# Kernel tuning notes

Measured on AMD Instinct MI355X. Metric: run time of the kernel, lower is better.

Reference implementation:

```python
import jax, jax.numpy as jnp
import numpy as np

N = 2_097_152   # batched ODE RHS evaluation points
T = 10_000      # forcing time-series length (days)
H = 16          # MLP hidden width


def _step(x):
    # smooth Heaviside used throughout EXP-Hydro
    return (jnp.tanh(5.0 * x) + 1.0) * 0.5


def _mlp(x, W1, b1, W2, b2, W3, b3):
    h = jnp.tanh(x @ W1 + b1)
    h = jnp.tanh(h @ W2 + b2)
    return (h @ W3 + b3)[..., 0]


def setup_inputs() -> dict:
    key = jax.random.key(0)
    ks = jax.random.split(key, 16)
    ts = jnp.arange(T, dtype=jnp.float32)
    inp = {
        "t": jax.random.uniform(ks[0], (N,), jnp.float32) * (T - 1),
        "S_snow": jax.random.uniform(ks[1], (N,), jnp.float32) * 50.0,
        "S_water": jax.random.uniform(ks[2], (N,), jnp.float32) * 1000.0,
        "ts": ts,
        "precp_series": jax.random.uniform(ks[3], (T,), jnp.float32) * 20.0,
        "temp_series": jax.random.normal(ks[4], (T,), jnp.float32) * 10.0,
        "lday_series": 0.3 + 0.4 * jax.random.uniform(ks[5], (T,), jnp.float32),
        "etW1": jax.random.normal(ks[6], (3, H), jnp.float32) * (1.0 / np.sqrt(3)),
        "etb1": jnp.zeros((H,), jnp.float32),
        "etW2": jax.random.normal(ks[7], (H, H), jnp.float32) * (1.0 / np.sqrt(H)),
        "etb2": jnp.zeros((H,), jnp.float32),
        "etW3": jax.random.normal(ks[8], (H, 1), jnp.float32) * (1.0 / np.sqrt(H)),
        "etb3": jnp.zeros((1,), jnp.float32),
        "qW1": jax.random.normal(ks[9], (2, H), jnp.float32) * (1.0 / np.sqrt(2)),
        "qb1": jnp.zeros((H,), jnp.float32),
        "qW2": jax.random.normal(ks[10], (H, H), jnp.float32) * (1.0 / np.sqrt(H)),
        "qb2": jnp.zeros((H,), jnp.float32),
        "qW3": jax.random.normal(ks[11], (H, 1), jnp.float32) * (1.0 / np.sqrt(H)),
        "qb3": jnp.zeros((1,), jnp.float32),
        "Df": jnp.float32(2.674),
        "Tmax": jnp.float32(0.176),
        "Tmin": jnp.float32(-2.093),
    }
    return inp


def reference(t, S_snow, S_water, ts, precp_series, temp_series, lday_series,
              etW1, etb1, etW2, etb2, etW3, etb3,
              qW1, qb1, qW2, qb2, qW3, qb3,
              Df, Tmax, Tmin):
    # linear interpolation of forcings at query times t  -> [N]
    precp = jnp.interp(t, ts, precp_series)
    temp = jnp.interp(t, ts, temp_series)
    lday = jnp.interp(t, ts, lday_series)

    ET = _mlp(jnp.stack([S_snow, S_water, temp], axis=-1),
              etW1, etb1, etW2, etb2, etW3, etb3)          # [N]
    Q = _mlp(jnp.stack([S_water, precp], axis=-1),
             qW1, qb1, qW2, qb2, qW3, qb3)                 # [N]

    # bucket physics (M / Ps / Pr with smooth step)
    melt = _step(temp - Tmax) * _step(S_snow) * jnp.minimum(S_snow, Df * (temp - Tmax))
    Ps = _step(Tmin - temp) * precp   # snowfall
    Pr = _step(temp - Tmin) * precp   # rainfall
    sw = _step(S_water)

    dS_1 = Ps - melt
    dS_2 = Pr + melt - sw * lday * jnp.exp(ET) - sw * jnp.exp(Q)
    return (dS_1, dS_2)
```

## Files before the change

kernel.cpp:

```cpp
#include <hip/hip_runtime.h>
#include <math.h>

#define BLOCK 256

typedef _Float16 half4v __attribute__((ext_vector_type(4)));
typedef float    float4v __attribute__((ext_vector_type(4)));

__device__ __forceinline__ float fast_tanh(float x) {
    float e = __expf(2.0f * x);
    float r = __builtin_amdgcn_rcpf(e + 1.0f);
    return 1.0f - 2.0f * r;
}

__device__ __forceinline__ float stepf(float x) {
    return (fast_tanh(5.0f * x) + 1.0f) * 0.5f;
}

__global__ __launch_bounds__(BLOCK) void pack_forcings_kernel(
    const float* __restrict__ precp_s, const float* __restrict__ temp_s,
    const float* __restrict__ lday_s, float4* __restrict__ F, int T)
{
    int i = blockIdx.x * BLOCK + threadIdx.x;
    if (i < T) F[i] = make_float4(precp_s[i], temp_s[i], lday_s[i], 0.0f);
}

__global__ __launch_bounds__(BLOCK, 4) void exphydro_mfma_kernel(
    const float* __restrict__ t, const float* __restrict__ S_snow,
    const float* __restrict__ S_water,
    const float4* __restrict__ F,
    const float* __restrict__ etW1, const float* __restrict__ etb1,
    const float* __restrict__ etW2, const float* __restrict__ etb2,
    const float* __restrict__ etW3, const float* __restrict__ etb3,
    const float* __restrict__ qW1, const float* __restrict__ qb1,
    const float* __restrict__ qW2, const float* __restrict__ qb2,
    const float* __restrict__ qW3, const float* __restrict__ qb3,
    const float* __restrict__ pDf, const float* __restrict__ pTmax,
    const float* __restrict__ pTmin,
    float* __restrict__ out, int N, int T)
{
    const int lane = threadIdx.x & 63;
    const int hi   = lane >> 4;
    const int m    = lane & 15;
    const int wave = threadIdx.x >> 6;
    const int base = blockIdx.x * BLOCK + wave * 64;
    const int p    = base + lane;
    const int pc   = (p < N) ? p : (N - 1);

    half4v A1et, A1q, A2et, A2q, A3et, A3q;
    float4v C2et, C2q;
    #pragma unroll
    for (int j = 0; j < 4; j++) {
        int k = 4 * hi + j;
        float w1e = (k < 3) ? etW1[k * 16 + m] : ((k == 3) ? etb1[m] : 0.0f);
        float w1q = (k < 2) ? qW1 [k * 16 + m] : ((k == 2) ? qb1 [m] : 0.0f);
        A1et[j] = (_Float16)w1e;
        A1q [j] = (_Float16)w1q;
        A2et[j] = (_Float16)etW2[k * 16 + m];
        A2q [j] = (_Float16)qW2 [k * 16 + m];
        A3et[j] = (_Float16)((m == 0) ? etW3[k] : 0.0f);
        A3q [j] = (_Float16)((m == 0) ? qW3 [k] : 0.0f);
        C2et[j] = etb2[4 * hi + j];
        C2q [j] = qb2 [4 * hi + j];
    }

    const float Df   = pDf[0];
    const float Tmax = pTmax[0];
    const float Tmin = pTmin[0];
    const float b3et = etb3[0];
    const float b3q  = qb3[0];
    const float tmaxf = (float)(T - 1);
    const int   imax  = T - 2;

    float tv    = t[pc];
    float ssnow = S_snow[pc];
    float swat  = S_water[pc];

    float tc = fminf(fmaxf(tv, 0.0f), tmaxf);
    int i0 = (int)tc;
    i0 = (i0 > imax) ? imax : i0;
    float fr = tc - (float)i0;
    float4 f0 = F[i0];
    float4 f1 = F[i0 + 1];
    float precp = fmaf(fr, f1.x - f0.x, f0.x);
    float temp  = fmaf(fr, f1.y - f0.y, f0.y);
    float lday  = fmaf(fr, f1.z - f0.z, f0.z);

    const float4v zero4 = {0.0f, 0.0f, 0.0f, 0.0f};
    float et4[4], q4[4];

    #pragma unroll
    for (int g = 0; g < 4; g++) {
        const int src = (g << 4) | m;
        float ss = __shfl(ssnow, src, 64);
        float sw = __shfl(swat,  src, 64);
        float tp = __shfl(temp,  src, 64);
        float pr = __shfl(precp, src, 64);

        half4v B1et, B1q;
        B1et[0] = (_Float16)ss;  B1et[1] = (_Float16)sw;
        B1et[2] = (_Float16)tp;  B1et[3] = (_Float16)1.0f;
        B1q [0] = (_Float16)sw;  B1q [1] = (_Float16)pr;
        B1q [2] = (_Float16)1.0f; B1q[3] = (_Float16)0.0f;

        float4v d1e = __builtin_amdgcn_mfma_f32_16x16x16f16(A1et, B1et, zero4, 0, 0, 0);
        float4v d1q = __builtin_amdgcn_mfma_f32_16x16x16f16(A1q,  B1q,  zero4, 0, 0, 0);

        half4v B2et, B2q;
        #pragma unroll
        for (int r = 0; r < 4; r++) B2et[r] = (_Float16)fast_tanh(d1e[r]);
        #pragma unroll
        for (int r = 0; r < 4; r++) B2q [r] = (_Float16)fast_tanh(d1q[r]);

        float4v d2e = __builtin_amdgcn_mfma_f32_16x16x16f16(A2et, B2et, C2et, 0, 0, 0);
        float4v d2q = __builtin_amdgcn_mfma_f32_16x16x16f16(A2q,  B2q,  C2q,  0, 0, 0);

        half4v B3et, B3q;
        #pragma unroll
        for (int r = 0; r < 4; r++) B3et[r] = (_Float16)fast_tanh(d2e[r]);
        #pragma unroll
        for (int r = 0; r < 4; r++) B3q [r] = (_Float16)fast_tanh(d2q[r]);

        float4v d3e = __builtin_amdgcn_mfma_f32_16x16x16f16(A3et, B3et, zero4, 0, 0, 0);
        float4v d3q = __builtin_amdgcn_mfma_f32_16x16x16f16(A3q,  B3q,  zero4, 0, 0, 0);

        et4[g] = d3e[0];
        q4 [g] = d3q[0];
    }

    float e0 = __shfl(et4[0], m, 64);
    float e1 = __shfl(et4[1], m, 64);
    float e2 = __shfl(et4[2], m, 64);
    float e3 = __shfl(et4[3], m, 64);
    float q0 = __shfl(q4[0], m, 64);
    float q1 = __shfl(q4[1], m, 64);
    float q2 = __shfl(q4[2], m, 64);
    float q3 = __shfl(q4[3], m, 64);
    float e01 = (lane & 16) ? e1 : e0;
    float e23 = (lane & 16) ? e3 : e2;
    float ET  = ((lane & 32) ? e23 : e01) + b3et;
    float q01 = (lane & 16) ? q1 : q0;
    float q23 = (lane & 16) ? q3 : q2;
    float Q   = ((lane & 32) ? q23 : q01) + b3q;

    float dT      = temp - Tmax;
    float melt    = stepf(dT) * stepf(ssnow) * fminf(ssnow, Df * dT);
    float st_snow = stepf(Tmin - temp);
    float Ps      = st_snow * precp;
    float Pr      = (1.0f - st_snow) * precp;
    float sw01    = stepf(swat);

    float dS1 = Ps - melt;
    float dS2 = Pr + melt - sw01 * (lday * __expf(ET) + __expf(Q));

    if (p < N) {
        out[p]     = dS1;
        out[N + p] = dS2;
    }
}

extern "C" void kernel_launch(void* const* d_in, const int* in_sizes, int n_in,
                              void* d_out, int out_size, void* d_ws, size_t ws_size,
                              hipStream_t stream) {
    const float* t        = (const float*)d_in[0];
    const float* S_snow   = (const float*)d_in[1];
    const float* S_water  = (const float*)d_in[2];
    const float* precp_s  = (const float*)d_in[4];
    const float* temp_s   = (const float*)d_in[5];
    const float* lday_s   = (const float*)d_in[6];
    const float* etW1     = (const float*)d_in[7];
    const float* etb1     = (const float*)d_in[8];
    const float* etW2     = (const float*)d_in[9];
    const float* etb2     = (const float*)d_in[10];
    const float* etW3     = (const float*)d_in[11];
    const float* etb3     = (const float*)d_in[12];
    const float* qW1      = (const float*)d_in[13];
    const float* qb1      = (const float*)d_in[14];
    const float* qW2      = (const float*)d_in[15];
    const float* qb2      = (const float*)d_in[16];
    const float* qW3      = (const float*)d_in[17];
    const float* qb3      = (const float*)d_in[18];
    const float* pDf      = (const float*)d_in[19];
    const float* pTmax    = (const float*)d_in[20];
    const float* pTmin    = (const float*)d_in[21];

    int N = in_sizes[0];
    int T = in_sizes[3];
    float* out = (float*)d_out;
    float4* F = (float4*)d_ws;

    pack_forcings_kernel<<<(T + BLOCK - 1) / BLOCK, BLOCK, 0, stream>>>(
        precp_s, temp_s, lday_s, F, T);

    exphydro_mfma_kernel<<<(N + BLOCK - 1) / BLOCK, BLOCK, 0, stream>>>(
        t, S_snow, S_water, F,
        etW1, etb1, etW2, etb2, etW3, etb3,
        qW1, qb1, qW2, qb2, qW3, qb3,
        pDf, pTmax, pTmin, out, N, T);
}
```

Measured before the change: 49.31 us.

## Use packed fp16 polynomial tanh and broadcast layer-3 weights to drop shuffles

Replaces the exp+rcp tanh with a clamped odd polynomial evaluated in packed fp16 vectors, for both the MLP activations and the smooth step functions. Inputs are packed to fp16 pairs before the wave shuffles, which halves the shuffle count. The layer-3 weights are broadcast across all MFMA rows and the bias is folded into the accumulator, so every lane receives its output directly and the final gather shuffles go away. The risk is accuracy: the fp16 polynomial with clamp at ±3 approximates tanh less closely, which matters most for the step functions on large physical inputs.

```diff
diff --git a/kernel.cpp b/kernel.cpp
--- a/kernel.cpp
+++ b/kernel.cpp
@@ -3,17 +3,51 @@
 
 #define BLOCK 256
 
+typedef _Float16 half2v __attribute__((ext_vector_type(2)));
 typedef _Float16 half4v __attribute__((ext_vector_type(4)));
 typedef float    float4v __attribute__((ext_vector_type(4)));
 
-__device__ __forceinline__ float fast_tanh(float x) {
-    float e = __expf(2.0f * x);
-    float r = __builtin_amdgcn_rcpf(e + 1.0f);
-    return 1.0f - 2.0f * r;
-}
-
-__device__ __forceinline__ float stepf(float x) {
-    return (fast_tanh(5.0f * x) + 1.0f) * 0.5f;
+__device__ __forceinline__ half2v cvt_pk_h2(float a, float b) {
+    return __builtin_bit_cast(half2v, __builtin_amdgcn_cvt_pkrtz(a, b));
+}
+
+#define H4(x) {(_Float16)(x), (_Float16)(x), (_Float16)(x), (_Float16)(x)}
+
+__device__ __forceinline__ half4v tanh_pk4(half4v x) {
+    const half4v c5 = H4(-3.71625e-05f);
+    const half4v c4 = H4( 1.09648e-03f);
+    const half4v c3 = H4(-1.288264e-02f);
+    const half4v c2 = H4( 7.941906e-02f);
+    const half4v c1 = H4(-3.0042735e-01f);
+    const half4v c0 = H4( 9.9607644e-01f);
+    const half4v hi = H4( 3.0f);
+    const half4v lo = H4(-3.0f);
+    half4v t = __builtin_elementwise_min(__builtin_elementwise_max(x, lo), hi);
+    half4v s = t * t;
+#if __has_builtin(__builtin_elementwise_fma)
+    half4v p = __builtin_elementwise_fma(c5, s, c4);
+    p = __builtin_elementwise_fma(p, s, c3);
+    p = __builtin_elementwise_fma(p, s, c2);
+    p = __builtin_elementwise_fma(p, s, c1);
+    p = __builtin_elementwise_fma(p, s, c0);
+#else
+    half4v p = c5 * s + c4;
+    p = p * s + c3;
+    p = p * s + c2;
+    p = p * s + c1;
+    p = p * s + c0;
+#endif
+    return t * p;
+}
+
+__device__ __forceinline__ half4v pk4_from_f32(float a, float b, float c, float d) {
+    half2v lo = cvt_pk_h2(a, b);
+    half2v hi = cvt_pk_h2(c, d);
+    return __builtin_shufflevector(lo, hi, 0, 1, 2, 3);
+}
+
+__device__ __forceinline__ half4v act4(float4v d) {
+    return tanh_pk4(pk4_from_f32(d[0], d[1], d[2], d[3]));
 }
 
 __global__ __launch_bounds__(BLOCK) void pack_forcings_kernel(
@@ -47,7 +81,7 @@
     const int pc   = (p < N) ? p : (N - 1);
 
     half4v A1et, A1q, A2et, A2q, A3et, A3q;
-    float4v C2et, C2q;
+    float4v C2et, C2q, C3et, C3q;
     #pragma unroll
     for (int j = 0; j < 4; j++) {
         int k = 4 * hi + j;
@@ -57,17 +91,17 @@
         A1q [j] = (_Float16)w1q;
         A2et[j] = (_Float16)etW2[k * 16 + m];
         A2q [j] = (_Float16)qW2 [k * 16 + m];
-        A3et[j] = (_Float16)((m == 0) ? etW3[k] : 0.0f);
-        A3q [j] = (_Float16)((m == 0) ? qW3 [k] : 0.0f);
+        A3et[j] = (_Float16)etW3[k];
+        A3q [j] = (_Float16)qW3 [k];
         C2et[j] = etb2[4 * hi + j];
         C2q [j] = qb2 [4 * hi + j];
+        C3et[j] = etb3[0];
+        C3q [j] = qb3 [0];
     }
 
     const float Df   = pDf[0];
     const float Tmax = pTmax[0];
     const float Tmin = pTmin[0];
-    const float b3et = etb3[0];
-    const float b3q  = qb3[0];
     const float tmaxf = (float)(T - 1);
     const int   imax  = T - 2;
 
@@ -85,69 +119,67 @@
     float temp  = fmaf(fr, f1.y - f0.y, f0.y);
     float lday  = fmaf(fr, f1.z - f0.z, f0.z);
 
+    half2v my01 = cvt_pk_h2(ssnow, swat);
+    half2v my23 = cvt_pk_h2(temp, precp);
+    int i01 = __builtin_bit_cast(int, my01);
+    int i23 = __builtin_bit_cast(int, my23);
+
     const float4v zero4 = {0.0f, 0.0f, 0.0f, 0.0f};
-    float et4[4], q4[4];
+    const _Float16 oneh = (_Float16)1.0f;
+    const _Float16 zerh = (_Float16)0.0f;
+    float et0, et1, et2, et3, q0, q1, q2, q3;
 
     #pragma unroll
     for (int g = 0; g < 4; g++) {
         const int src = (g << 4) | m;
-        float ss = __shfl(ssnow, src, 64);
-        float sw = __shfl(swat,  src, 64);
-        float tp = __shfl(temp,  src, 64);
-        float pr = __shfl(precp, src, 64);
-
-        half4v B1et, B1q;
-        B1et[0] = (_Float16)ss;  B1et[1] = (_Float16)sw;
-        B1et[2] = (_Float16)tp;  B1et[3] = (_Float16)1.0f;
-        B1q [0] = (_Float16)sw;  B1q [1] = (_Float16)pr;
-        B1q [2] = (_Float16)1.0f; B1q[3] = (_Float16)0.0f;
+        int j01 = __shfl(i01, src, 64);
+        int j23 = __shfl(i23, src, 64);
+        half2v a01 = __builtin_bit_cast(half2v, j01);
+        half2v a23 = __builtin_bit_cast(half2v, j23);
+
+        half4v B1et = {a01[0], a01[1], a23[0], oneh};
+        half4v B1q  = {a01[1], a23[1], oneh,  zerh};
 
         float4v d1e = __builtin_amdgcn_mfma_f32_16x16x16f16(A1et, B1et, zero4, 0, 0, 0);
         float4v d1q = __builtin_amdgcn_mfma_f32_16x16x16f16(A1q,  B1q,  zero4, 0, 0, 0);
 
-        half4v B2et, B2q;
-        #pragma unroll
-        for (int r = 0; r < 4; r++) B2et[r] = (_Float16)fast_tanh(d1e[r]);
-        #pragma unroll
-        for (int r = 0; r < 4; r++) B2q [r] = (_Float16)fast_tanh(d1q[r]);
+        half4v B2et = act4(d1e);
+        half4v B2q  = act4(d1q);
 
         float4v d2e = __builtin_amdgcn_mfma_f32_16x16x16f16(A2et, B2et, C2et, 0, 0, 0);
         float4v d2q = __builtin_amdgcn_mfma_f32_16x16x16f16(A2q,  B2q,  C2q,  0, 0, 0);
 
-        half4v B3et, B3q;
-        #pragma unroll
-        for (int r = 0; r < 4; r++) B3et[r] = (_Float16)fast_tanh(d2e[r]);
-        #pragma unroll
-        for (int r = 0; r < 4; r++) B3q [r] = (_Float16)fast_tanh(d2q[r]);
-
-        float4v d3e = __builtin_amdgcn_mfma_f32_16x16x16f16(A3et, B3et, zero4, 0, 0, 0);
-        float4v d3q = __builtin_amdgcn_mfma_f32_16x16x16f16(A3q,  B3q,  zero4, 0, 0, 0);
-
-        et4[g] = d3e[0];
-        q4 [g] = d3q[0];
+        half4v B3et = act4(d2e);
+        half4v B3q  = act4(d2q);
+
+        float4v d3e = __builtin_amdgcn_mfma_f32_16x16x16f16(A3et, B3et, C3et, 0, 0, 0);
+        float4v d3q = __builtin_amdgcn_mfma_f32_16x16x16f16(A3q,  B3q,  C3q,  0, 0, 0);
+
+        if (g == 0) { et0 = d3e[0]; q0 = d3q[0]; }
+        if (g == 1) { et1 = d3e[0]; q1 = d3q[0]; }
+        if (g == 2) { et2 = d3e[0]; q2 = d3q[0]; }
+        if (g == 3) { et3 = d3e[0]; q3 = d3q[0]; }
     }
 
-    float e0 = __shfl(et4[0], m, 64);
-    float e1 = __shfl(et4[1], m, 64);
-    float e2 = __shfl(et4[2], m, 64);
-    float e3 = __shfl(et4[3], m, 64);
-    float q0 = __shfl(q4[0], m, 64);
-    float q1 = __shfl(q4[1], m, 64);
-    float q2 = __shfl(q4[2], m, 64);
-    float q3 = __shfl(q4[3], m, 64);
-    float e01 = (lane & 16) ? e1 : e0;
-    float e23 = (lane & 16) ? e3 : e2;
-    float ET  = ((lane & 32) ? e23 : e01) + b3et;
+    float e01 = (lane & 16) ? et1 : et0;
+    float e23 = (lane & 16) ? et3 : et2;
+    float ET  = (lane & 32) ? e23 : e01;
     float q01 = (lane & 16) ? q1 : q0;
     float q23 = (lane & 16) ? q3 : q2;
-    float Q   = ((lane & 32) ? q23 : q01) + b3q;
-
-    float dT      = temp - Tmax;
-    float melt    = stepf(dT) * stepf(ssnow) * fminf(ssnow, Df * dT);
-    float st_snow = stepf(Tmin - temp);
-    float Ps      = st_snow * precp;
-    float Pr      = (1.0f - st_snow) * precp;
-    float sw01    = stepf(swat);
+    float Q   = (lane & 32) ? q23 : q01;
+
+    float dT = temp - Tmax;
+    half4v sargs = pk4_from_f32(5.0f * dT, 5.0f * ssnow,
+                                5.0f * (Tmin - temp), 5.0f * swat);
+    half4v th = tanh_pk4(sargs);
+    float stepA  = fmaf(0.5f, (float)th[0], 0.5f);
+    float stepSn = fmaf(0.5f, (float)th[1], 0.5f);
+    float stepPs = fmaf(0.5f, (float)th[2], 0.5f);
+    float sw01   = fmaf(0.5f, (float)th[3], 0.5f);
+
+    float melt = stepA * stepSn * fminf(ssnow, Df * dT);
+    float Ps   = stepPs * precp;
+    float Pr   = (1.0f - stepPs) * precp;
 
     float dS1 = Ps - melt;
     float dS2 = Pr + melt - sw01 * (lday * __expf(ET) + __expf(Q));
```

Measured after the change: 42.64 us. 1.16x faster.
